# Kernel optimization log

Measured on AMD Instinct MI355X. Metric: run time of the kernel, lower is better.

Reference implementation:

```python
import jax, jax.numpy as jnp
import numpy as np

D_MODEL, D_STATE, D_CONV, EXPAND = 2048, 16, 4, 2
D_INNER = EXPAND * D_MODEL            # 4096
DT_RANK = -(-D_MODEL // 16)           # 128
B_SZ, L = 2, 1024


def setup_inputs() -> dict:
    key = jax.random.key(0)
    ks = jax.random.split(key, 10)
    s = 0.02
    return {
        "hidden_states": jax.random.normal(ks[0], (B_SZ, L, D_MODEL), jnp.float32),
        "in_proj_w": jax.random.normal(ks[1], (2 * D_INNER, D_MODEL), jnp.float32) * s,
        "conv_w": jax.random.normal(ks[2], (D_INNER, D_CONV), jnp.float32) * 0.1,
        "conv_b": jax.random.normal(ks[3], (D_INNER,), jnp.float32) * 0.1,
        "x_proj_w": jax.random.normal(ks[4], (DT_RANK + 2 * D_STATE, D_INNER), jnp.float32) * s,
        "dt_proj_w": jax.random.normal(ks[5], (D_INNER, DT_RANK), jnp.float32) * s,
        "dt_proj_b": jax.random.normal(ks[6], (D_INNER,), jnp.float32) * 0.1 - 4.0,
        "A": -jax.random.uniform(ks[7], (D_INNER, D_STATE), jnp.float32, 1.0, 16.0),
        "D": jnp.ones((D_INNER,), jnp.float32),
        "out_proj_w": jax.random.normal(ks[8], (D_MODEL, D_INNER), jnp.float32) * s,
    }


def _mamba_forward(hidden_states, in_proj_w, conv_w, conv_b, x_proj_w,
                   dt_proj_w, dt_proj_b, A, D, out_proj_w):
    # in_proj: [B,L,d_model] -> [B,L,2*d_inner]; chunk into x and gate
    proj = jnp.einsum('bld,ed->ble', hidden_states, in_proj_w)
    x, gate = jnp.split(proj, 2, axis=-1)            # each [B,L,d_inner]

    # depthwise causal conv1d over time + SiLU
    xc = x.transpose(0, 2, 1)                        # [B,d_inner,L]
    xc = jax.lax.conv_general_dilated(
        xc, conv_w[:, None, :],                      # kernel [d_inner,1,d_conv]
        window_strides=(1,), padding=[(D_CONV - 1, 0)],
        feature_group_count=D_INNER,
        dimension_numbers=('NCH', 'OIH', 'NCH'))
    xc = jax.nn.silu(xc + conv_b[None, :, None])
    xt = xc.transpose(0, 2, 1)                       # [B,L,d_inner]

    # x_proj -> (dt_rank, d_state, d_state)
    ssm = jnp.einsum('bld,ed->ble', xt, x_proj_w)
    ts, Bm, Cm = jnp.split(ssm, [DT_RANK, DT_RANK + D_STATE], axis=-1)
    dt = jnp.einsum('blr,dr->bld', ts, dt_proj_w)    # dt_proj (skip_bias_add)
    dt = jax.nn.softplus(dt + dt_proj_b)             # delta_softplus with bias

    # selective scan over time
    def step(state, inp):
        dt_t, x_t, B_t, C_t = inp                    # [B,di],[B,di],[B,ds],[B,ds]
        dA = jnp.exp(dt_t[..., None] * A)            # [B,d_inner,d_state]
        dBx = dt_t[..., None] * B_t[:, None, :] * x_t[..., None]
        state = state * dA + dBx
        y = jnp.einsum('bds,bs->bd', state, C_t)
        return state, y

    xs = (dt.transpose(1, 0, 2), xt.transpose(1, 0, 2),
          Bm.transpose(1, 0, 2), Cm.transpose(1, 0, 2))
    state0 = jnp.zeros((hidden_states.shape[0], D_INNER, D_STATE), jnp.float32)
    _, ys = jax.lax.scan(step, state0, xs)           # [L,B,d_inner]
    y = ys.transpose(1, 0, 2) + xt * D               # D skip connection
    y = y * jax.nn.silu(gate)                        # gating (z in selective scan)

    return jnp.einsum('bld,ed->ble', y, out_proj_w)  # out_proj -> [B,L,d_model]


def reference(hidden_states, in_proj_w, conv_w, conv_b, x_proj_w,
              dt_proj_w, dt_proj_b, A, D, out_proj_w):
    return _mamba_forward(hidden_states, in_proj_w, conv_w, conv_b, x_proj_w,
                          dt_proj_w, dt_proj_b, A, D, out_proj_w)
```

## Files before the change

kernel.cpp:

```cpp
#include <hip/hip_runtime.h>
#include <hip/hip_bf16.h>
#include <math.h>

#define B_SZ    2
#define LSEQ    1024
#define D_MODEL 2048
#define D_INNER 4096
#define D_STATE 16
#define DT_RANK 128
#define M_TOK   (B_SZ * LSEQ)
#define NCHUNK  16
#define LCHUNK  (LSEQ / NCHUNK)

typedef __attribute__((ext_vector_type(8))) short bf16x8;
typedef __attribute__((ext_vector_type(4))) float f32x4;

__device__ __forceinline__ float softplusf_(float x) {
    return fmaxf(x, 0.f) + log1pf(expf(-fabsf(x)));
}
__device__ __forceinline__ unsigned f2bf(float f) {
    union { float f; unsigned u; } v; v.f = f;
    const unsigned u = v.u;
    return (u + 0x7fffu + ((u >> 16) & 1u)) >> 16;
}
__device__ __forceinline__ float bf2f(unsigned u) {
    union { unsigned u; float f; } v; v.u = u << 16; return v.f;
}
__device__ __forceinline__ void gload16(const void* g, void* lds) {
    __builtin_amdgcn_global_load_lds(
        (const __attribute__((address_space(1))) void*)g,
        (__attribute__((address_space(3))) void*)lds, 16, 0, 0);
}

__global__ __launch_bounds__(512, 4)
void gemm_bf16_bt(const ushort* __restrict__ A, int lda,
                  const ushort* __restrict__ B, int ldb,
                  void* __restrict__ Cv, int ldc,
                  void* __restrict__ Cv2,
                  const float* __restrict__ bias,
                  int M, int N, int K, int epi, size_t zstride)
{
    __shared__ ushort As[2][128 * 64];
    __shared__ ushort Bs[2][128 * 64];
    const int t    = threadIdx.x;
    const int bm   = blockIdx.y << 7, bn = blockIdx.x << 7;
    const int wave = t >> 6, lane = t & 63;
    const int wr   = (wave >> 2) << 6;
    const int wc   = (wave & 3) << 5;
    const int lr   = lane & 15, lh = lane >> 4;
    const int kper  = K / gridDim.z;
    const int kbase = blockIdx.z * kper;
    const int nkt   = kper >> 6;

    const ushort* ga[2]; const ushort* gb[2];
    int ldof[2];
#pragma unroll
    for (int it = 0; it < 2; ++it) {
        const int seg = wave + (it << 3);
        const int row = (seg << 3) + (lane >> 3);
        const int jj  = (lane & 7) ^ ((lane >> 3) & 7);
        ga[it] = A + (size_t)(bm + row) * lda + kbase + jj * 8;
        int gn = bn + row; gn = gn < N ? gn : N - 1;
        gb[it] = B + (size_t)gn * ldb + kbase + jj * 8;
        ldof[it] = seg << 9;
    }

#define STAGE(bsel) do {                                                \
    _Pragma("unroll")                                                   \
    for (int it = 0; it < 2; ++it) {                                    \
        gload16(ga[it], &As[bsel][ldof[it]]);                           \
        gload16(gb[it], &Bs[bsel][ldof[it]]);                           \
        ga[it] += 64; gb[it] += 64;                                     \
    }                                                                   \
} while (0)

    f32x4 acc[4][2];
#pragma unroll
    for (int i = 0; i < 4; ++i)
#pragma unroll
        for (int j = 0; j < 2; ++j) {
            acc[i][j][0] = 0.f; acc[i][j][1] = 0.f;
            acc[i][j][2] = 0.f; acc[i][j][3] = 0.f;
        }

    STAGE(0);
    for (int kt = 0; kt < nkt; ++kt) {
        const int cur = kt & 1;
        if (kt + 1 < nkt) {
            STAGE(cur ^ 1);
            asm volatile("s_waitcnt vmcnt(4)" ::: "memory");
        } else {
            asm volatile("s_waitcnt vmcnt(0)" ::: "memory");
        }
        __builtin_amdgcn_s_barrier();
        __builtin_amdgcn_sched_barrier(0);

        const char* Ab = (const char*)As[cur];
        const char* Bb = (const char*)Bs[cur];
#pragma unroll
        for (int kk = 0; kk < 2; ++kk) {
            bf16x8 af[4], bf[2];
#pragma unroll
            for (int mi = 0; mi < 4; ++mi) {
                const int row = wr + (mi << 4) + lr;
                const int ch  = ((kk << 2) + lh) ^ (row & 7);
                af[mi] = *(const bf16x8*)(Ab + row * 128 + (ch << 4));
            }
#pragma unroll
            for (int nj = 0; nj < 2; ++nj) {
                const int row = wc + (nj << 4) + lr;
                const int ch  = ((kk << 2) + lh) ^ (row & 7);
                bf[nj] = *(const bf16x8*)(Bb + row * 128 + (ch << 4));
            }
#pragma unroll
            for (int mi = 0; mi < 4; ++mi)
#pragma unroll
                for (int nj = 0; nj < 2; ++nj)
                    acc[mi][nj] = __builtin_amdgcn_mfma_f32_16x16x32_bf16(
                        af[mi], bf[nj], acc[mi][nj], 0, 0, 0);
        }
        __builtin_amdgcn_s_barrier();
        __builtin_amdgcn_sched_barrier(0);
    }
#undef STAGE

    float*  C  = (float*)Cv + (size_t)blockIdx.z * zstride;
    ushort* Cb = (ushort*)Cv;
    ushort* C2 = (ushort*)Cv2;
#pragma unroll
    for (int mi = 0; mi < 4; ++mi) {
#pragma unroll
        for (int nj = 0; nj < 2; ++nj) {
            const int col  = bn + wc + (nj << 4) + lr;
            const int row0 = bm + wr + (mi << 4) + (lh << 2);
            if (col < N) {
#pragma unroll
                for (int r = 0; r < 4; ++r) {
                    const float v = acc[mi][nj][r];
                    if (epi == 0) {
                        C[(size_t)(row0 + r) * ldc + col] = v;
                    } else if (epi == 1) {
                        Cb[(size_t)(row0 + r) * ldc + col] =
                            (ushort)f2bf(softplusf_(v + bias[col]));
                    } else {
                        if (col < D_INNER)
                            Cb[(size_t)(row0 + r) * ldc + col] = (ushort)f2bf(v);
                        else
                            C2[(size_t)(row0 + r) * ldc + (col - D_INNER)] = (ushort)f2bf(v);
                    }
                }
            }
        }
    }
}

__global__ __launch_bounds__(256)
void cvt_bf16(const float* __restrict__ in, ushort* __restrict__ out, int n8)
{
    for (int i = blockIdx.x * 256 + threadIdx.x; i < n8; i += gridDim.x * 256) {
        const float4 v0 = ((const float4*)in)[i * 2];
        const float4 v1 = ((const float4*)in)[i * 2 + 1];
        int4 p;
        p.x = (int)(f2bf(v0.x) | (f2bf(v0.y) << 16));
        p.y = (int)(f2bf(v0.z) | (f2bf(v0.w) << 16));
        p.z = (int)(f2bf(v1.x) | (f2bf(v1.y) << 16));
        p.w = (int)(f2bf(v1.z) | (f2bf(v1.w) << 16));
        ((int4*)out)[i] = p;
    }
}

__global__ __launch_bounds__(256)
void reduce_out(const float* __restrict__ part, float* __restrict__ out, int n4)
{
    for (int i = blockIdx.x * 256 + threadIdx.x; i < n4; i += gridDim.x * 256) {
        const float4 a = ((const float4*)part)[i];
        const float4 b = ((const float4*)(part + (size_t)M_TOK * D_MODEL))[i];
        ((float4*)out)[i] = make_float4(a.x + b.x, a.y + b.y, a.z + b.z, a.w + b.w);
    }
}

__global__ __launch_bounds__(256)
void conv_silu_k(const ushort* __restrict__ xraw,
                 const float* __restrict__ cw,
                 const float* __restrict__ cb,
                 ushort* __restrict__ xb)
{
    const int d  = (blockIdx.x << 8) + threadIdx.x;
    const int m0 = blockIdx.y << 6;
    const int l0 = m0 & (LSEQ - 1);
    const float4 w = *(const float4*)&cw[d << 2];
    const float bias = cb[d];
    float x3 = 0.f, x2 = 0.f, x1 = 0.f;
    if (l0 > 0) {
        x3 = bf2f(xraw[(size_t)(m0 - 3) * D_INNER + d]);
        x2 = bf2f(xraw[(size_t)(m0 - 2) * D_INNER + d]);
        x1 = bf2f(xraw[(size_t)(m0 - 1) * D_INNER + d]);
    }
#pragma unroll 4
    for (int i = 0; i < 64; ++i) {
        const size_t m = (size_t)m0 + i;
        const float x0 = bf2f(xraw[m * D_INNER + d]);
        float acc = bias;
        acc = fmaf(w.x, x3, acc);
        acc = fmaf(w.y, x2, acc);
        acc = fmaf(w.z, x1, acc);
        acc = fmaf(w.w, x0, acc);
        const float sg = 1.f / (1.f + expf(-acc));
        xb[m * D_INNER + d] = (ushort)f2bf(acc * sg);
        x3 = x2; x2 = x1; x1 = x0;
    }
}

__global__ __launch_bounds__(256)
void reduce_ssm(const float* __restrict__ part,
                float* __restrict__ ssmf, ushort* __restrict__ ssmb)
{
    const int i = blockIdx.x * 256 + threadIdx.x;
    float v = 0.f;
#pragma unroll
    for (int z = 0; z < 8; ++z) v += part[(size_t)z * (M_TOK * 160) + i];
    ssmf[i] = v;
    ssmb[i] = (ushort)f2bf(v);
}

__global__ __launch_bounds__(256)
void scan_pass1(const ushort* __restrict__ dtp,
                const ushort* __restrict__ xb,
                const float* __restrict__ ssm,
                const float* __restrict__ Ap,
                float* __restrict__ Pc, float* __restrict__ Qc)
{
    const int d = (blockIdx.x << 8) + threadIdx.x;
    const int c = blockIdx.y, b = blockIdx.z;
    float a[16];
    *(float4*)&a[0]  = *(const float4*)&Ap[d * 16];
    *(float4*)&a[4]  = *(const float4*)&Ap[d * 16 + 4];
    *(float4*)&a[8]  = *(const float4*)&Ap[d * 16 + 8];
    *(float4*)&a[12] = *(const float4*)&Ap[d * 16 + 12];
    float q[16];
#pragma unroll
    for (int s = 0; s < 16; ++s) q[s] = 0.f;
    float dtsum = 0.f;
    const size_t m0 = (size_t)b * LSEQ + (size_t)c * LCHUNK;
#pragma unroll 2
    for (int l = 0; l < LCHUNK; ++l) {
        const size_t m = m0 + l;
        const float dt = bf2f(dtp[m * D_INNER + d]);
        const float xv = bf2f(xb[m * D_INNER + d]);
        const float4 B0 = *(const float4*)&ssm[m * 160 + 128];
        const float4 B1 = *(const float4*)&ssm[m * 160 + 132];
        const float4 B2 = *(const float4*)&ssm[m * 160 + 136];
        const float4 B3 = *(const float4*)&ssm[m * 160 + 140];
        const float Bv[16] = {B0.x,B0.y,B0.z,B0.w, B1.x,B1.y,B1.z,B1.w,
                              B2.x,B2.y,B2.z,B2.w, B3.x,B3.y,B3.z,B3.w};
        const float t1 = dt * xv;
#pragma unroll
        for (int s = 0; s < 16; ++s) {
            const float dA = __expf(dt * a[s]);
            q[s] = fmaf(q[s], dA, t1 * Bv[s]);
        }
        dtsum += dt;
    }
    const size_t o = (((size_t)b * D_INNER + d) * NCHUNK + c) * D_STATE;
    float P[16];
#pragma unroll
    for (int s = 0; s < 16; ++s) P[s] = __expf(a[s] * dtsum);
#pragma unroll
    for (int s4 = 0; s4 < 4; ++s4) {
        *(float4*)&Pc[o + s4 * 4] = make_float4(P[s4*4], P[s4*4+1], P[s4*4+2], P[s4*4+3]);
        *(float4*)&Qc[o + s4 * 4] = make_float4(q[s4*4], q[s4*4+1], q[s4*4+2], q[s4*4+3]);
    }
}

__global__ __launch_bounds__(256)
void scan_pass2(const float* __restrict__ Pc, float* __restrict__ Qc)
{
    const int i = blockIdx.x * 256 + threadIdx.x;
    const size_t base = (size_t)(i >> 4) * (NCHUNK * D_STATE) + (i & 15);
    float st = 0.f;
#pragma unroll
    for (int c = 0; c < NCHUNK; ++c) {
        const float P = Pc[base + c * D_STATE];
        const float q = Qc[base + c * D_STATE];
        Qc[base + c * D_STATE] = st;
        st = fmaf(st, P, q);
    }
}

__global__ __launch_bounds__(256)
void scan_pass3(const ushort* __restrict__ dtp,
                ushort* __restrict__ xb,
                const ushort* __restrict__ gb,
                const float* __restrict__ ssm,
                const float* __restrict__ Ap,
                const float* __restrict__ Qc,
                const float* __restrict__ Dp)
{
    const int d = (blockIdx.x << 8) + threadIdx.x;
    const int c = blockIdx.y, b = blockIdx.z;
    float a[16], st[16];
    *(float4*)&a[0]  = *(const float4*)&Ap[d * 16];
    *(float4*)&a[4]  = *(const float4*)&Ap[d * 16 + 4];
    *(float4*)&a[8]  = *(const float4*)&Ap[d * 16 + 8];
    *(float4*)&a[12] = *(const float4*)&Ap[d * 16 + 12];
    const size_t qo = (((size_t)b * D_INNER + d) * NCHUNK + c) * D_STATE;
    *(float4*)&st[0]  = *(const float4*)&Qc[qo];
    *(float4*)&st[4]  = *(const float4*)&Qc[qo + 4];
    *(float4*)&st[8]  = *(const float4*)&Qc[qo + 8];
    *(float4*)&st[12] = *(const float4*)&Qc[qo + 12];
    const float Dd = Dp[d];
    const size_t m0 = (size_t)b * LSEQ + (size_t)c * LCHUNK;
#pragma unroll 2
    for (int l = 0; l < LCHUNK; ++l) {
        const size_t m = m0 + l;
        const float dt = bf2f(dtp[m * D_INNER + d]);
        const float xv = bf2f(xb[m * D_INNER + d]);
        const float gv = bf2f(gb[m * D_INNER + d]);
        const float4 B0 = *(const float4*)&ssm[m * 160 + 128];
        const float4 B1 = *(const float4*)&ssm[m * 160 + 132];
        const float4 B2 = *(const float4*)&ssm[m * 160 + 136];
        const float4 B3 = *(const float4*)&ssm[m * 160 + 140];
        const float4 C0 = *(const float4*)&ssm[m * 160 + 144];
        const float4 C1 = *(const float4*)&ssm[m * 160 + 148];
        const float4 C2 = *(const float4*)&ssm[m * 160 + 152];
        const float4 C3 = *(const float4*)&ssm[m * 160 + 156];
        const float Bv[16] = {B0.x,B0.y,B0.z,B0.w, B1.x,B1.y,B1.z,B1.w,
                              B2.x,B2.y,B2.z,B2.w, B3.x,B3.y,B3.z,B3.w};
        const float Cv[16] = {C0.x,C0.y,C0.z,C0.w, C1.x,C1.y,C1.z,C1.w,
                              C2.x,C2.y,C2.z,C2.w, C3.x,C3.y,C3.z,C3.w};
        const float t1 = dt * xv;
        float y = 0.f;
#pragma unroll
        for (int s = 0; s < 16; ++s) {
            const float dA = __expf(dt * a[s]);
            st[s] = fmaf(st[s], dA, t1 * Bv[s]);
            y = fmaf(st[s], Cv[s], y);
        }
        const float yg  = fmaf(Dd, xv, y);
        const float sig = 1.f / (1.f + expf(-gv));
        xb[m * D_INNER + d] = (ushort)f2bf(yg * (gv * sig));
    }
}

extern "C" void kernel_launch(void* const* d_in, const int* in_sizes, int n_in,
                              void* d_out, int out_size, void* d_ws, size_t ws_size,
                              hipStream_t stream)
{
    (void)in_sizes; (void)n_in; (void)out_size; (void)ws_size;
    const float* hs  = (const float*)d_in[0];
    const float* inw = (const float*)d_in[1];
    const float* cw  = (const float*)d_in[2];
    const float* cb  = (const float*)d_in[3];
    const float* xw  = (const float*)d_in[4];
    const float* dtw = (const float*)d_in[5];
    const float* dtb = (const float*)d_in[6];
    const float* Ap  = (const float*)d_in[7];
    const float* Dp  = (const float*)d_in[8];
    const float* ow  = (const float*)d_in[9];
    float* out = (float*)d_out;

    float*  ws    = (float*)d_ws;
    ushort* pg    = (ushort*)(ws + 0);
    ushort* xraw  = (ushort*)(ws + 4194304);
    ushort* xtb   = (ushort*)(ws + 8388608);
    float*  ssmf  = ws + 12582912;
    ushort* ssmb  = (ushort*)(ws + 12910592);
    ushort* xwb   = (ushort*)(ws + 13074432);
    ushort* dtwb  = (ushort*)(ws + 13402112);
    ushort* hsb   = (ushort*)(ws + 13664256);
    ushort* inwb  = (ushort*)(ws + 15761408);
    ushort* owb   = (ushort*)(ws + 15761408);
    float*  part  = ws + 19955712;
    ushort* dtb16 = (ushort*)(ws + 19955712);
    float*  Pc    = ws + 4194304;
    float*  Qc    = ws + 6291456;
    float*  opart = ws + 0;

    const dim3 blk(256);
    const dim3 blk512(512);

    cvt_bf16<<<dim3(1280), blk, 0, stream>>>(hs,  hsb,  524288);
    cvt_bf16<<<dim3(1280), blk, 0, stream>>>(inw, inwb, 2097152);
    cvt_bf16<<<dim3(1280), blk, 0, stream>>>(xw,  xwb,  81920);
    cvt_bf16<<<dim3(1280), blk, 0, stream>>>(dtw, dtwb, 65536);

    gemm_bf16_bt<<<dim3(64, 16, 1), blk512, 0, stream>>>(
        hsb, D_MODEL, inwb, D_MODEL, xraw, D_INNER, pg, nullptr,
        M_TOK, 2 * D_INNER, D_MODEL, 5, 0);

    cvt_bf16<<<dim3(1280), blk, 0, stream>>>(ow, owb, 1048576);

    conv_silu_k<<<dim3(16, 32), blk, 0, stream>>>(xraw, cw, cb, xtb);

    gemm_bf16_bt<<<dim3(2, 16, 8), blk512, 0, stream>>>(
        xtb, D_INNER, xwb, D_INNER, part, 160, nullptr, nullptr,
        M_TOK, 160, D_INNER, 0, (size_t)M_TOK * 160);
    reduce_ssm<<<dim3(1280), blk, 0, stream>>>(part, ssmf, ssmb);

    gemm_bf16_bt<<<dim3(32, 16, 1), blk512, 0, stream>>>(
        ssmb, 160, dtwb, DT_RANK, dtb16, D_INNER, nullptr, dtb,
        M_TOK, D_INNER, DT_RANK, 1, 0);

    scan_pass1<<<dim3(16, NCHUNK, B_SZ), blk, 0, stream>>>(dtb16, xtb, ssmf, Ap, Pc, Qc);
    scan_pass2<<<dim3((B_SZ * D_INNER * D_STATE) / 256), blk, 0, stream>>>(Pc, Qc);
    scan_pass3<<<dim3(16, NCHUNK, B_SZ), blk, 0, stream>>>(dtb16, xtb, pg, ssmf, Ap, Qc, Dp);

    gemm_bf16_bt<<<dim3(16, 16, 2), blk512, 0, stream>>>(
        xtb, D_INNER, owb, D_INNER, opart, D_MODEL, nullptr, nullptr,
        M_TOK, D_MODEL, D_INNER, 0, (size_t)M_TOK * D_MODEL);
    reduce_out<<<dim3(1024), blk, 0, stream>>>(opart, out, (M_TOK * D_MODEL) / 4);
}
```

Measured before the change: 324.1 us.

## Add 256x256 eight-phase pipelined GEMM for in_proj and out_proj

Result: faster. 307.3 us (-5.2%).

```diff
diff --git a/kernel.cpp b/kernel.cpp
--- a/kernel.cpp
+++ b/kernel.cpp
@@ -32,11 +32,178 @@
         (__attribute__((address_space(3))) void*)lds, 16, 0, 0);
 }
 
+__global__ __launch_bounds__(512, 2)
+void gemm256_8ph(const ushort* __restrict__ A, int lda,
+                 const ushort* __restrict__ B, int ldb,
+                 void* __restrict__ Cv, int ldc,
+                 void* __restrict__ Cv2,
+                 int K, int epi, size_t zstride)
+{
+    __shared__ ushort Lds[2][2][2][128 * 64];
+    const int t    = threadIdx.x;
+    const int bm   = blockIdx.y << 8, bn = blockIdx.x << 8;
+    const int wave = t >> 6, lane = t & 63;
+    const int wm   = wave >> 2;
+    const int wn   = wave & 3;
+    const int lr   = lane & 15, lh = lane >> 4;
+    const int kper  = K / gridDim.z;
+    const int kbase = blockIdx.z * kper;
+    const int nkt   = kper >> 6;
+
+    const ushort* gsA[2]; const ushort* gsB[2];
+    int dof[2];
+#pragma unroll
+    for (int it = 0; it < 2; ++it) {
+        const int flat = t + (it << 9);
+        const int row  = flat >> 3, j = flat & 7;
+        const int jj   = j ^ (row & 7);
+        gsA[it] = A + (size_t)(bm + row) * lda + kbase + jj * 8;
+        gsB[it] = B + (size_t)(bn + row) * ldb + kbase + jj * 8;
+        dof[it] = flat << 3;
+    }
+
+#define STG_A(half, kt, db) do {                                            \
+    _Pragma("unroll")                                                       \
+    for (int it = 0; it < 2; ++it)                                          \
+        gload16(gsA[it] + (size_t)((half) * 128) * lda + (kt) * 64,         \
+                &Lds[db][0][half][dof[it]]);                                \
+} while (0)
+#define STG_B(half, kt, db) do {                                            \
+    _Pragma("unroll")                                                       \
+    for (int it = 0; it < 2; ++it)                                          \
+        gload16(gsB[it] + (size_t)((half) * 128) * ldb + (kt) * 64,         \
+                &Lds[db][1][half][dof[it]]);                                \
+} while (0)
+#define RD_A(db, half) do {                                                 \
+    _Pragma("unroll")                                                       \
+    for (int mi = 0; mi < 4; ++mi)                                          \
+    _Pragma("unroll")                                                       \
+    for (int kk = 0; kk < 2; ++kk) {                                        \
+        const int row_ = wm * 64 + mi * 16 + lr;                            \
+        const int ch_  = ((kk << 2) + lh) ^ (row_ & 7);                     \
+        af[mi * 2 + kk] = *(const bf16x8*)((const char*)Lds[db][0][half]    \
+                             + row_ * 128 + (ch_ << 4));                    \
+    }                                                                       \
+} while (0)
+#define RD_B(db, half, dst) do {                                            \
+    _Pragma("unroll")                                                       \
+    for (int nj = 0; nj < 2; ++nj)                                          \
+    _Pragma("unroll")                                                       \
+    for (int kk = 0; kk < 2; ++kk) {                                        \
+        const int row_ = wn * 32 + nj * 16 + lr;                            \
+        const int ch_  = ((kk << 2) + lh) ^ (row_ & 7);                     \
+        dst[nj * 2 + kk] = *(const bf16x8*)((const char*)Lds[db][1][half]   \
+                             + row_ * 128 + (ch_ << 4));                    \
+    }                                                                       \
+} while (0)
+#define MFMA_Q(q, bfx) do {                                                 \
+    _Pragma("unroll")                                                       \
+    for (int mi = 0; mi < 4; ++mi)                                          \
+    _Pragma("unroll")                                                       \
+    for (int nj = 0; nj < 2; ++nj)                                          \
+    _Pragma("unroll")                                                       \
+    for (int kk = 0; kk < 2; ++kk)                                          \
+        acc[q][mi][nj] = __builtin_amdgcn_mfma_f32_16x16x32_bf16(           \
+            af[mi * 2 + kk], bfx[nj * 2 + kk], acc[q][mi][nj], 0, 0, 0);    \
+} while (0)
+#define PH_PRE()  __builtin_amdgcn_s_barrier();                             \
+                  asm volatile("s_waitcnt lgkmcnt(0)" ::: "memory");        \
+                  __builtin_amdgcn_sched_barrier(0);                        \
+                  __builtin_amdgcn_s_setprio(1)
+#define PH_POST() __builtin_amdgcn_s_setprio(0);                            \
+                  __builtin_amdgcn_s_barrier();                             \
+                  __builtin_amdgcn_sched_barrier(0)
+
+    f32x4 acc[4][4][2];
+#pragma unroll
+    for (int q = 0; q < 4; ++q)
+#pragma unroll
+        for (int i = 0; i < 4; ++i)
+#pragma unroll
+            for (int j = 0; j < 2; ++j) {
+                acc[q][i][j][0] = 0.f; acc[q][i][j][1] = 0.f;
+                acc[q][i][j][2] = 0.f; acc[q][i][j][3] = 0.f;
+            }
+
+    bf16x8 af[8], bf0[4], bf1[4];
+
+    STG_A(0, 0, 0); STG_B(0, 0, 0); STG_B(1, 0, 0); STG_A(1, 0, 0);
+    if (nkt > 1) { STG_A(0, 1, 1); STG_B(0, 1, 1); STG_B(1, 1, 1); }
+    asm volatile("s_waitcnt vmcnt(6)" ::: "memory");
+    __builtin_amdgcn_s_barrier();
+    __builtin_amdgcn_sched_barrier(0);
+
+    for (int kt = 0; kt < nkt; ++kt) {
+        const int db = kt & 1;
+        RD_A(db, 0); RD_B(db, 0, bf0);
+        if (kt + 1 < nkt) STG_A(1, kt + 1, db ^ 1);
+        PH_PRE();
+        MFMA_Q(0, bf0);
+        PH_POST();
+        RD_B(db, 1, bf1);
+        if (kt + 2 < nkt) STG_A(0, kt + 2, db);
+        PH_PRE();
+        MFMA_Q(1, bf1);
+        PH_POST();
+        RD_A(db, 1);
+        if (kt + 2 < nkt) STG_B(0, kt + 2, db);
+        PH_PRE();
+        MFMA_Q(2, bf1);
+        PH_POST();
+        if (kt + 2 < nkt) STG_B(1, kt + 2, db);
+        PH_PRE();
+        MFMA_Q(3, bf0);
+        __builtin_amdgcn_s_setprio(0);
+        if (kt + 2 >= nkt) {
+            asm volatile("s_waitcnt vmcnt(0)" ::: "memory");
+        } else {
+            asm volatile("s_waitcnt vmcnt(6)" ::: "memory");
+        }
+        __builtin_amdgcn_s_barrier();
+        __builtin_amdgcn_sched_barrier(0);
+    }
+#undef STG_A
+#undef STG_B
+#undef RD_A
+#undef RD_B
+#undef MFMA_Q
+#undef PH_PRE
+#undef PH_POST
+
+    float*  C  = (float*)Cv + (size_t)blockIdx.z * zstride;
+    ushort* Cb = (ushort*)Cv;
+    ushort* C2 = (ushort*)Cv2;
+#pragma unroll
+    for (int q = 0; q < 4; ++q) {
+        const int mh = q >> 1;
+        const int nh = (q == 1 || q == 2) ? 1 : 0;
+#pragma unroll
+        for (int mi = 0; mi < 4; ++mi) {
+#pragma unroll
+            for (int nj = 0; nj < 2; ++nj) {
+                const int col  = bn + nh * 128 + wn * 32 + nj * 16 + lr;
+                const int row0 = bm + mh * 128 + wm * 64 + mi * 16 + (lh << 2);
+#pragma unroll
+                for (int r = 0; r < 4; ++r) {
+                    const float v = acc[q][mi][nj][r];
+                    if (epi == 0) {
+                        C[(size_t)(row0 + r) * ldc + col] = v;
+                    } else {
+                        if (col < D_INNER)
+                            Cb[(size_t)(row0 + r) * ldc + col] = (ushort)f2bf(v);
+                        else
+                            C2[(size_t)(row0 + r) * ldc + (col - D_INNER)] = (ushort)f2bf(v);
+                    }
+                }
+            }
+        }
+    }
+}
+
 __global__ __launch_bounds__(512, 4)
 void gemm_bf16_bt(const ushort* __restrict__ A, int lda,
                   const ushort* __restrict__ B, int ldb,
                   void* __restrict__ Cv, int ldc,
-                  void* __restrict__ Cv2,
                   const float* __restrict__ bias,
                   int M, int N, int K, int epi, size_t zstride)
 {
@@ -126,7 +293,6 @@
 
     float*  C  = (float*)Cv + (size_t)blockIdx.z * zstride;
     ushort* Cb = (ushort*)Cv;
-    ushort* C2 = (ushort*)Cv2;
 #pragma unroll
     for (int mi = 0; mi < 4; ++mi) {
 #pragma unroll
@@ -137,17 +303,11 @@
 #pragma unroll
                 for (int r = 0; r < 4; ++r) {
                     const float v = acc[mi][nj][r];
-                    if (epi == 0) {
+                    if (epi == 0)
                         C[(size_t)(row0 + r) * ldc + col] = v;
-                    } else if (epi == 1) {
+                    else
                         Cb[(size_t)(row0 + r) * ldc + col] =
                             (ushort)f2bf(softplusf_(v + bias[col]));
-                    } else {
-                        if (col < D_INNER)
-                            Cb[(size_t)(row0 + r) * ldc + col] = (ushort)f2bf(v);
-                        else
-                            C2[(size_t)(row0 + r) * ldc + (col - D_INNER)] = (ushort)f2bf(v);
-                    }
                 }
             }
         }
@@ -170,12 +330,18 @@
 }
 
 __global__ __launch_bounds__(256)
-void reduce_out(const float* __restrict__ part, float* __restrict__ out, int n4)
-{
+void reduce_out4(const float* __restrict__ part, float* __restrict__ out, int n4)
+{
+    const int stride = M_TOK * D_MODEL / 4;
     for (int i = blockIdx.x * 256 + threadIdx.x; i < n4; i += gridDim.x * 256) {
         const float4 a = ((const float4*)part)[i];
-        const float4 b = ((const float4*)(part + (size_t)M_TOK * D_MODEL))[i];
-        ((float4*)out)[i] = make_float4(a.x + b.x, a.y + b.y, a.z + b.z, a.w + b.w);
+        const float4 b = ((const float4*)part)[i + stride];
+        const float4 c = ((const float4*)part)[i + 2 * stride];
+        const float4 d = ((const float4*)part)[i + 3 * stride];
+        ((float4*)out)[i] = make_float4(a.x + b.x + c.x + d.x,
+                                        a.y + b.y + c.y + d.y,
+                                        a.z + b.z + c.z + d.z,
+                                        a.w + b.w + c.w + d.w);
     }
 }
 
@@ -360,53 +526,52 @@
     float* out = (float*)d_out;
 
     float*  ws    = (float*)d_ws;
-    ushort* pg    = (ushort*)(ws + 0);
-    ushort* xraw  = (ushort*)(ws + 4194304);
-    ushort* xtb   = (ushort*)(ws + 8388608);
-    float*  ssmf  = ws + 12582912;
-    ushort* ssmb  = (ushort*)(ws + 12910592);
-    ushort* xwb   = (ushort*)(ws + 13074432);
-    ushort* dtwb  = (ushort*)(ws + 13402112);
-    ushort* hsb   = (ushort*)(ws + 13664256);
-    ushort* inwb  = (ushort*)(ws + 15761408);
-    ushort* owb   = (ushort*)(ws + 15761408);
-    float*  part  = ws + 19955712;
-    ushort* dtb16 = (ushort*)(ws + 19955712);
-    float*  Pc    = ws + 4194304;
-    float*  Qc    = ws + 6291456;
-    float*  opart = ws + 0;
+    float*  P     = ws;
+    ushort* hsb   = (ushort*)(ws + 0);
+    ushort* inwb  = (ushort*)(ws + 2097152);
+    ushort* dtb16 = (ushort*)(ws + 0);
+    ushort* xwb   = (ushort*)(ws + 4194304);
+    ushort* dtwb  = (ushort*)(ws + 4521984);
+    float*  ssmf  = ws + 4784128;
+    ushort* ssmb  = (ushort*)(ws + 5111808);
+    float*  part  = ws + 5275648;
+    float*  Pc    = ws + 5275648;
+    float*  Qc    = ws + 7372800;
+    ushort* pg    = (ushort*)(ws + 10485760);
+    ushort* xtb   = (ushort*)(ws + 16777216);
+    ushort* xraw  = (ushort*)(ws + 20971520);
+    ushort* owb   = (ushort*)(ws + 20971520);
 
     const dim3 blk(256);
     const dim3 blk512(512);
 
     cvt_bf16<<<dim3(1280), blk, 0, stream>>>(hs,  hsb,  524288);
     cvt_bf16<<<dim3(1280), blk, 0, stream>>>(inw, inwb, 2097152);
+
+    gemm256_8ph<<<dim3(32, 8, 1), blk512, 0, stream>>>(
+        hsb, D_MODEL, inwb, D_MODEL, xraw, D_INNER, pg, D_MODEL, 5, 0);
+
+    conv_silu_k<<<dim3(16, 32), blk, 0, stream>>>(xraw, cw, cb, xtb);
+
+    cvt_bf16<<<dim3(1280), blk, 0, stream>>>(ow,  owb, 1048576);
     cvt_bf16<<<dim3(1280), blk, 0, stream>>>(xw,  xwb,  81920);
     cvt_bf16<<<dim3(1280), blk, 0, stream>>>(dtw, dtwb, 65536);
 
-    gemm_bf16_bt<<<dim3(64, 16, 1), blk512, 0, stream>>>(
-        hsb, D_MODEL, inwb, D_MODEL, xraw, D_INNER, pg, nullptr,
-        M_TOK, 2 * D_INNER, D_MODEL, 5, 0);
-
-    cvt_bf16<<<dim3(1280), blk, 0, stream>>>(ow, owb, 1048576);
-
-    conv_silu_k<<<dim3(16, 32), blk, 0, stream>>>(xraw, cw, cb, xtb);
-
     gemm_bf16_bt<<<dim3(2, 16, 8), blk512, 0, stream>>>(
-        xtb, D_INNER, xwb, D_INNER, part, 160, nullptr, nullptr,
+        xtb, D_INNER, xwb, D_INNER, part, 160, nullptr,
         M_TOK, 160, D_INNER, 0, (size_t)M_TOK * 160);
     reduce_ssm<<<dim3(1280), blk, 0, stream>>>(part, ssmf, ssmb);
 
     gemm_bf16_bt<<<dim3(32, 16, 1), blk512, 0, stream>>>(
-        ssmb, 160, dtwb, DT_RANK, dtb16, D_INNER, nullptr, dtb,
+        ssmb, 160, dtwb, DT_RANK, dtb16, D_INNER, dtb,
         M_TOK, D_INNER, DT_RANK, 1, 0);
 
     scan_pass1<<<dim3(16, NCHUNK, B_SZ), blk, 0, stream>>>(dtb16, xtb, ssmf, Ap, Pc, Qc);
     scan_pass2<<<dim3((B_SZ * D_INNER * D_STATE) / 256), blk, 0, stream>>>(Pc, Qc);
     scan_pass3<<<dim3(16, NCHUNK, B_SZ), blk, 0, stream>>>(dtb16, xtb, pg, ssmf, Ap, Qc, Dp);
 
-    gemm_bf16_bt<<<dim3(16, 16, 2), blk512, 0, stream>>>(
-        xtb, D_INNER, owb, D_INNER, opart, D_MODEL, nullptr, nullptr,
-        M_TOK, D_MODEL, D_INNER, 0, (size_t)M_TOK * D_MODEL);
-    reduce_out<<<dim3(1024), blk, 0, stream>>>(opart, out, (M_TOK * D_MODEL) / 4);
-}
+    gemm256_8ph<<<dim3(8, 8, 4), blk512, 0, stream>>>(
+        xtb, D_INNER, owb, D_INNER, P, D_MODEL, nullptr,
+        D_INNER, 0, (size_t)M_TOK * D_MODEL);
+    reduce_out4<<<dim3(1024), blk, 0, stream>>>(P, out, (M_TOK * D_MODEL) / 4);
+}
```
